# Kernel tuning notes

Hardware: AMD Instinct MI355X
Metric: run time of the kernel (lower is better)

Reference implementation:

```python
import jax, jax.numpy as jnp
import numpy as np

D_MODEL = 2048
NUM_HEADS = 16
D_K = D_MODEL // NUM_HEADS


def _xavier(key, shape):
    # xavier_uniform_ for a (fan_in, fan_out) matrix
    limit = np.sqrt(6.0 / (shape[0] + shape[1]))
    return jax.random.uniform(key, shape, dtype=jnp.float32, minval=-limit, maxval=limit)


def setup_inputs() -> dict:
    key = jax.random.key(0)
    kx, kq, kk, kv, ko = jax.random.split(key, 5)
    x = jax.random.normal(kx, (4, 2048, D_MODEL), dtype=jnp.float32)
    return {
        "x": x,
        "w_q": _xavier(kq, (D_MODEL, D_MODEL)),
        "w_k": _xavier(kk, (D_MODEL, D_MODEL)),
        "w_v": _xavier(kv, (D_MODEL, D_MODEL)),
        "w_o": _xavier(ko, (D_MODEL, D_MODEL)),
    }


def _split_heads(t):
    b, s, _ = t.shape
    return t.reshape(b, s, NUM_HEADS, D_K).transpose(0, 2, 1, 3)  # [b,h,s,dk]


def reference(x, w_q, w_k, w_v, w_o):
    q = _split_heads(x @ w_q)
    k = _split_heads(x @ w_k)
    v = _split_heads(x @ w_v)
    scale = 1.0 / np.sqrt(D_K).astype(np.float32)
    scores = jnp.einsum("bhqd,bhkd->bhqk", q, k) * scale
    attn = jax.nn.softmax(scores, axis=-1)
    out = jnp.einsum("bhqk,bhkd->bhqd", attn, v)  # [b,h,s,dk]
    b, h, s, dk = out.shape
    out = out.transpose(0, 2, 1, 3).reshape(b, s, h * dk)
    return out @ w_o
```

## Files before the change

### kernel.cpp

```cpp
#include <hip/hip_runtime.h>
#include <hip/hip_bf16.h>

typedef __attribute__((ext_vector_type(8))) __bf16 bf16x8;
typedef __attribute__((ext_vector_type(4))) float f32x4;
typedef __attribute__((ext_vector_type(16))) float f32x16;
typedef __attribute__((ext_vector_type(8))) unsigned short u16x8;
typedef unsigned short u16;

#define DEVINL static __device__ __forceinline__

namespace {
constexpr int kB = 4;
constexpr int kS = 2048;
constexpr int kDM = 2048;
constexpr int kH = 16;
constexpr int kDK = 128;
constexpr int kM = kB * kS;
constexpr int kNQKV = 3 * kDM;
constexpr float kE2 = 0.08838834764831845f * 1.44269504088896f;
}

DEVINL u16 f2bf(float f) {
  __hip_bfloat16 h = __float2bfloat16(f);
  return __builtin_bit_cast(u16, h);
}

#if __has_builtin(__builtin_amdgcn_exp2f)
DEVINL float exp2_fast(float x) { return __builtin_amdgcn_exp2f(x); }
#else
DEVINL float exp2_fast(float x) { return exp2f(x); }
#endif

#define GLOAD16(gp, lp) \
  __builtin_amdgcn_global_load_lds((const __attribute__((address_space(1))) void*)(gp), \
                                   (__attribute__((address_space(3))) void*)(lp), 16, 0, 0)

DEVINL bf16x8 lds_frag(const u16* p) { return *reinterpret_cast<const bf16x8*>(p); }

DEVINL f32x4 MFMA16x16(bf16x8 a, bf16x8 b, f32x4 c) {
  return __builtin_amdgcn_mfma_f32_16x16x32_bf16(a, b, c, 0, 0, 0);
}

struct TrueT { static constexpr bool value = true; };
struct FalseT { static constexpr bool value = false; };

__global__ __launch_bounds__(256) void cast_x_kernel(const float* __restrict__ x,
                                                     u16* __restrict__ o, int n4) {
  int i = blockIdx.x * 256 + threadIdx.x;
  if (i >= n4) return;
  float4 v = reinterpret_cast<const float4*>(x)[i];
  ushort4 r;
  r.x = f2bf(v.x); r.y = f2bf(v.y); r.z = f2bf(v.z); r.w = f2bf(v.w);
  reinterpret_cast<ushort4*>(o)[i] = r;
}

__global__ __launch_bounds__(256) void transpose_w_kernel(const float* __restrict__ w0,
    const float* __restrict__ w1, const float* __restrict__ w2, const float* __restrict__ w3,
    u16* __restrict__ wtcat, u16* __restrict__ wot) {
  const float* src = (blockIdx.z == 0) ? w0 : (blockIdx.z == 1) ? w1
                    : (blockIdx.z == 2) ? w2 : w3;
  u16* dst = (blockIdx.z < 3) ? (wtcat + (size_t)blockIdx.z * kDM * kDM) : wot;
  __shared__ float tile[32][33];
  int n0 = blockIdx.x * 32, k0 = blockIdx.y * 32;
  int tx = threadIdx.x, ty = threadIdx.y;
#pragma unroll
  for (int i = 0; i < 4; ++i)
    tile[ty + i * 8][tx] = src[(size_t)(k0 + ty + i * 8) * kDM + n0 + tx];
  __syncthreads();
#pragma unroll
  for (int i = 0; i < 4; ++i)
    dst[(size_t)(n0 + ty + i * 8) * kDM + k0 + tx] = f2bf(tile[tx][ty + i * 8]);
}

DEVINL void cstore(float* p, float v) { *p = v; }
DEVINL void cstore(u16* p, float v) { *p = f2bf(v); }

#define PH_BEGIN()                                     \
  __builtin_amdgcn_sched_barrier(0);                   \
  __builtin_amdgcn_s_barrier();                        \
  asm volatile("s_waitcnt lgkmcnt(0)" ::: "memory");   \
  __builtin_amdgcn_sched_barrier(0);                   \
  __builtin_amdgcn_s_setprio(1)

#define PH_END()                                       \
  __builtin_amdgcn_s_setprio(0);                       \
  __builtin_amdgcn_sched_barrier(0)

#define GATE4() \
  asm volatile("s_waitcnt vmcnt(4)" ::: "memory");     \
  __builtin_amdgcn_sched_barrier(0)

#define GATE0() \
  asm volatile("s_waitcnt vmcnt(0)" ::: "memory");     \
  __builtin_amdgcn_sched_barrier(0)

#define RD_A(SB, MQ, DST)                                             \
  do {                                                                \
    _Pragma("unroll") for (int mf = 0; mf < 4; ++mf) {                \
      const u16* p_ = (SB) + (awrow + (MQ) * 64 + mf * 16) * 64;      \
      DST[mf * 2 + 0] = lds_frag(p_ + g0);                            \
      DST[mf * 2 + 1] = lds_frag(p_ + g1);                            \
    }                                                                 \
  } while (0)

#define RD_BH(SB, NH)                                                 \
  do {                                                                \
    _Pragma("unroll") for (int nf = 0; nf < 2; ++nf) {                \
      const u16* p_ = (SB) + (bwrow + (NH) * 32 + nf * 16) * 64;      \
      b[(NH) * 4 + nf * 2 + 0] = lds_frag(p_ + g0);                   \
      b[(NH) * 4 + nf * 2 + 1] = lds_frag(p_ + g1);                   \
    }                                                                 \
  } while (0)

#define MMQ(MQ, NH, AF)                                               \
  do {                                                                \
    _Pragma("unroll") for (int mf = 0; mf < 4; ++mf)                  \
      _Pragma("unroll") for (int nf = 0; nf < 2; ++nf) {              \
        f32x4 t_ = acc[(MQ) * 4 + mf][(NH) * 2 + nf];                 \
        t_ = MFMA16x16(AF[mf * 2 + 0], b[(NH) * 4 + nf * 2 + 0], t_); \
        t_ = MFMA16x16(AF[mf * 2 + 1], b[(NH) * 4 + nf * 2 + 1], t_); \
        acc[(MQ) * 4 + mf][(NH) * 2 + nf] = t_;                       \
      }                                                               \
  } while (0)

#define STG_A(buf, R0, kt) \
  GLOAD16(baseA + (size_t)(R0) * lda + (size_t)(kt) * 64, ldsA + (buf) * 16384 + (R0) * 64)
#define STG_B(buf, R0, kt) \
  GLOAD16(baseB + (size_t)(R0) * ldb + (size_t)(kt) * 64, ldsB + (buf) * 16384 + (R0) * 64)

template <typename CT, bool WRITEV>
__global__ __launch_bounds__(512, 2) void gemm256_kernel(const u16* __restrict__ A,
    const u16* __restrict__ Bt, CT* __restrict__ C, u16* __restrict__ Vt,
    int K, int lda, int ldb, int ldc) {
  __shared__ __align__(16) u16 sA[2][16384];
  __shared__ __align__(16) u16 sB[2][16384];
  const int tid = threadIdx.x;
  const int lane = tid & 63, wid = tid >> 6;
  const int r15 = lane & 15, hi = lane >> 4;
  const int wm = wid >> 2, wn = wid & 3;

  const int gx = gridDim.x, nwg = gx * gridDim.y;
  const int orig = blockIdx.y * gx + blockIdx.x;
  const int wg = (orig & 7) * (nwg >> 3) + (orig >> 3);
  const int n0 = (wg % gx) * 256;
  const int m0 = (wg / gx) * 256;

  const int NT = K >> 6;
  const int NITER = NT >> 1;

  const int rc = tid >> 3;
  const int cg = (tid & 7) ^ (rc & 7);
  const u16* baseA = A + (size_t)(m0 + rc) * lda + cg * 8;
  const u16* baseB = Bt + (size_t)(n0 + rc) * ldb + cg * 8;
  u16* ldsA = &sA[0][0] + rc * 64 + (tid & 7) * 8;
  u16* ldsB = &sB[0][0] + rc * 64 + (tid & 7) * 8;

  const int sw = r15 & 7;
  const int g0 = (hi ^ sw) * 8;
  const int g1 = ((4 + hi) ^ sw) * 8;
  const int awrow = wm * 128 + r15;
  const int bwrow = wn * 64 + r15;
  const u16* sA0 = &sA[0][0]; const u16* sA1 = &sA[1][0];
  const u16* sB0 = &sB[0][0]; const u16* sB1 = &sB[1][0];

  f32x4 acc[8][4] = {};
  bf16x8 aE[8], aO[8], b[8];

  STG_A(0, 0, 0); STG_A(0, 64, 0); STG_A(0, 128, 0); STG_A(0, 192, 0);
  STG_B(0, 0, 0); STG_B(0, 64, 0); STG_B(0, 128, 0); STG_B(0, 192, 0);
  STG_A(1, 0, 1); STG_A(1, 128, 1);
  STG_B(1, 0, 1); STG_B(1, 64, 1); STG_B(1, 128, 1); STG_B(1, 192, 1);
  asm volatile("s_waitcnt vmcnt(6)" ::: "memory");
  __builtin_amdgcn_sched_barrier(0);
  __builtin_amdgcn_s_barrier();
  RD_A(sA0, 0, aE); RD_BH(sB0, 0);

  int kb = 0;
  auto iter = [&](auto lastc) {
    constexpr bool L = decltype(lastc)::value;
    const int kO = kb + 1, k2 = kb + 2, k3 = kb + 3;
    PH_BEGIN();
    RD_BH(sB0, 1);
    MMQ(0, 0, aE);
    PH_END();
    STG_A(1, 64, kO); STG_A(1, 192, kO);
    PH_BEGIN();
    RD_A(sA0, 1, aO);
    MMQ(0, 1, aE);
    PH_END();
    if constexpr (!L) { STG_A(0, 0, k2); STG_A(0, 128, k2); }
    PH_BEGIN();
    MMQ(1, 0, aO);
    PH_END();
    if constexpr (!L) { STG_B(0, 0, k2); STG_B(0, 64, k2); GATE4(); }
    else              { GATE0(); }
    PH_BEGIN();
    RD_A(sA1, 0, aE); RD_BH(sB1, 0);
    MMQ(1, 1, aO);
    PH_END();
    if constexpr (!L) { STG_B(0, 128, k2); STG_B(0, 192, k2); }
    PH_BEGIN();
    RD_BH(sB1, 1);
    MMQ(0, 0, aE);
    PH_END();
    if constexpr (!L) { STG_A(0, 64, k2); STG_A(0, 192, k2); }
    PH_BEGIN();
    RD_A(sA1, 1, aO);
    MMQ(0, 1, aE);
    PH_END();
    if constexpr (!L) { STG_A(1, 0, k3); STG_A(1, 128, k3); }
    PH_BEGIN();
    MMQ(1, 0, aO);
    PH_END();
    if constexpr (!L) { STG_B(1, 0, k3); STG_B(1, 64, k3); GATE4(); }
    else              { GATE0(); }
    PH_BEGIN();
    if constexpr (!L) { RD_A(sA0, 0, aE); RD_BH(sB0, 0); }
    MMQ(1, 1, aO);
    PH_END();
    if constexpr (!L) { STG_B(1, 128, k3); STG_B(1, 192, k3); }
    kb += 2;
  };
  for (int i = 0; i < NITER - 1; ++i) iter(FalseT{});
  iter(TrueT{});

  if constexpr (WRITEV) {
    if (n0 >= 2 * kDM) {
      const int hswap = ((hi & 1) << 1) | (hi >> 1);
#pragma unroll
      for (int im = 0; im < 8; ++im) {
        const int m_base = m0 + wm * 128 + im * 16;
        const int bq = m_base >> 11;
        const int sp = (m_base & (kS - 1)) + hswap * 4;
#pragma unroll
        for (int in = 0; in < 4; ++in) {
          const int c = n0 - 2 * kDM + wn * 64 + in * 16 + r15;
          const int hh = c >> 7, dd = c & 127;
          u16* dst = Vt + ((size_t)((bq * kH + hh) * kDK + dd)) * kS + sp;
          ushort4 pk;
          pk.x = f2bf(acc[im][in][0]); pk.y = f2bf(acc[im][in][1]);
          pk.z = f2bf(acc[im][in][2]); pk.w = f2bf(acc[im][in][3]);
          *reinterpret_cast<ushort4*>(dst) = pk;
        }
      }
      return;
    }
  }
  const size_t crow0 = (size_t)(m0 + wm * 128 + hi * 4);
  const int col0 = n0 + wn * 64 + r15;
#pragma unroll
  for (int im = 0; im < 8; ++im)
#pragma unroll
    for (int in = 0; in < 4; ++in)
#pragma unroll
      for (int r = 0; r < 4; ++r)
        cstore(&C[(crow0 + im * 16 + r) * ldc + col0 + in * 16], acc[im][in][r]);
}

__global__ __launch_bounds__(256, 2) void attn_kernel(const u16* __restrict__ qkv,
    const u16* __restrict__ vt, u16* __restrict__ attn_out) {
  __shared__ __align__(16) u16 lds[2][16384];
  const int tid = threadIdx.x;
  const int lane = tid & 63, wid = tid >> 6;
  const int l31 = lane & 31, hi5 = lane >> 5;
  const int q0 = blockIdx.x * 128, h = blockIdx.y, b = blockIdx.z;
  const int bh = b * kH + h;

  const int krow = tid >> 4, kg = tid & 15;
  const u16* kp = qkv + (size_t)(b * kS + krow) * kNQKV + kDM + h * kDK
                  + (size_t)((kg ^ (krow & 7)) * 8);
  const int vrow = tid >> 3, vg = tid & 7;
  const u16* vp = vt + (size_t)(bh * kDK + vrow) * kS + (size_t)((vg ^ (vrow & 7)) * 8);

  auto stage_kv = [&](u16* dst) {
#pragma unroll
    for (int i = 0; i < 4; ++i)
      GLOAD16(kp + (size_t)i * 16 * kNQKV, dst + (tid + 256 * i) * 8);
#pragma unroll
    for (int i = 0; i < 4; ++i)
      GLOAD16(vp + (size_t)i * 32 * kS, dst + 8192 + (tid + 256 * i) * 8);
    kp += (size_t)64 * kNQKV;
    vp += 64;
  };

#pragma unroll
  for (int i = 0; i < 8; ++i) {
    int row = (tid >> 4) + 16 * i;
    GLOAD16(qkv + (size_t)(b * kS + q0 + row) * kNQKV + h * kDK
                + (size_t)(((tid & 15) ^ (row & 7)) * 8),
            (u16*)lds[1] + (tid + 256 * i) * 8);
  }
  stage_kv(lds[0]);
  __syncthreads();

  bf16x8 qf[8];
  {
    const int qrow = wid * 32 + l31;
    const u16* qb = (const u16*)lds[1];
#pragma unroll
    for (int ds = 0; ds < 8; ++ds) {
      int slot = (ds * 2 + hi5) ^ (qrow & 7);
      qf[ds] = lds_frag(&qb[qrow * 128 + slot * 8]);
    }
  }
  __syncthreads();

  f32x16 o[4] = {};
  float mi = -1e30f, li = 0.f;
  int cur = 0;

  for (int t = 0; t < kS / 64; ++t) {
    if (t < kS / 64 - 1) stage_kv(lds[cur ^ 1]);

    const u16* Kb = (const u16*)lds[cur];
    const u16* Vb = Kb + 8192;

    f32x16 s0 = {}, s1 = {};
    const int kr = l31;
#pragma unroll
    for (int ds = 0; ds < 8; ++ds) {
      int slot = ((ds * 2 + hi5) ^ (kr & 7)) * 8;
      bf16x8 k0 = lds_frag(&Kb[kr * 128 + slot]);
      bf16x8 k1 = lds_frag(&Kb[(32 + kr) * 128 + slot]);
      s0 = __builtin_amdgcn_mfma_f32_32x32x16_bf16(k0, qf[ds], s0, 0, 0, 0);
      s1 = __builtin_amdgcn_mfma_f32_32x32x16_bf16(k1, qf[ds], s1, 0, 0, 0);
    }

    float mx = s0[0];
#pragma unroll
    for (int r = 1; r < 16; ++r) mx = fmaxf(mx, s0[r]);
#pragma unroll
    for (int r = 0; r < 16; ++r) mx = fmaxf(mx, s1[r]);
    mx = fmaxf(mx, __shfl_xor(mx, 32));
    float mc = mx * kE2;
    if (__any(mc > mi + 8.0f)) {
      float mn = fmaxf(mi, mc);
      float corr = exp2_fast(mi - mn);
      mi = mn;
      li *= corr;
#pragma unroll
      for (int r = 0; r < 16; ++r) {
        float c = __shfl(corr, (r & 3) + 8 * (r >> 2) + 4 * hi5);
        o[0][r] *= c; o[1][r] *= c; o[2][r] *= c; o[3][r] *= c;
      }
    }
    float p0[16], p1[16];
    float rs = 0.f;
#pragma unroll
    for (int r = 0; r < 16; ++r) { p0[r] = exp2_fast(s0[r] * kE2 - mi); rs += p0[r]; }
#pragma unroll
    for (int r = 0; r < 16; ++r) { p1[r] = exp2_fast(s1[r] * kE2 - mi); rs += p1[r]; }
    rs += __shfl_xor(rs, 32);
    li += rs;

    u16x8 pw0, pw1, pw2, pw3;
#pragma unroll
    for (int r = 0; r < 8; ++r) {
      pw0[r] = f2bf(p0[r]);
      pw1[r] = f2bf(p0[r + 8]);
      pw2[r] = f2bf(p1[r]);
      pw3[r] = f2bf(p1[r + 8]);
    }
    bf16x8 pa[4] = {__builtin_bit_cast(bf16x8, pw0), __builtin_bit_cast(bf16x8, pw1),
                    __builtin_bit_cast(bf16x8, pw2), __builtin_bit_cast(bf16x8, pw3)};

#pragma unroll
    for (int dt = 0; dt < 4; ++dt) {
      const int row = dt * 32 + l31;
      const int rs8 = row & 7;
#pragma unroll
      for (int ks = 0; ks < 4; ++ks) {
        bf16x8 bv = lds_frag(&Vb[row * 64 + ((ks * 2 + hi5) ^ rs8) * 8]);
        o[dt] = __builtin_amdgcn_mfma_f32_32x32x16_bf16(pa[ks], bv, o[dt], 0, 0, 0);
      }
    }

    __syncthreads();
    cur ^= 1;
  }

  float rli = 1.0f / li;
  const size_t obase = (size_t)(b * kS + q0 + wid * 32) * kDM + h * kDK + l31;
#pragma unroll
  for (int r = 0; r < 16; ++r) {
    int ql = (r & 3) + 8 * (r >> 2) + 4 * hi5;
    float w = __shfl(rli, ql);
#pragma unroll
    for (int dt = 0; dt < 4; ++dt)
      attn_out[obase + (size_t)ql * kDM + dt * 32] = f2bf(o[dt][r] * w);
  }
}

extern "C" void kernel_launch(void* const* d_in, const int* in_sizes, int n_in,
                              void* d_out, int out_size, void* d_ws, size_t ws_size,
                              hipStream_t stream) {
  (void)in_sizes; (void)n_in; (void)out_size; (void)ws_size;
  const float* x  = (const float*)d_in[0];
  const float* wq = (const float*)d_in[1];
  const float* wk = (const float*)d_in[2];
  const float* wv = (const float*)d_in[3];
  const float* wo = (const float*)d_in[4];

  char* p = (char*)d_ws;
  u16* xb   = (u16*)p; p += (size_t)kM * kDM * 2;
  u16* wtc  = (u16*)p; p += (size_t)kNQKV * kDM * 2;
  u16* wot  = (u16*)p; p += (size_t)kDM * kDM * 2;
  u16* qkvb = (u16*)p; p += (size_t)kM * kNQKV * 2;
  u16* vtb  = (u16*)p; p += (size_t)kB * kH * kDK * kS * 2;
  u16* aob  = xb;

  int n4 = kM * kDM / 4;
  cast_x_kernel<<<(n4 + 255) / 256, 256, 0, stream>>>(x, xb, n4);
  transpose_w_kernel<<<dim3(kDM / 32, kDM / 32, 4), dim3(32, 8), 0, stream>>>(
      wq, wk, wv, wo, wtc, wot);
  gemm256_kernel<u16, true><<<dim3(kNQKV / 256, kM / 256), 512, 0, stream>>>(
      xb, wtc, qkvb, vtb, kDM, kDM, kDM, kNQKV);
  attn_kernel<<<dim3(kS / 128, kH, kB), 256, 0, stream>>>(qkvb, vtb, aob);
  gemm256_kernel<float, false><<<dim3(kDM / 256, kM / 256), 512, 0, stream>>>(
      aob, wot, (float*)d_out, nullptr, kDM, kDM, kDM, kDM);
}
```

Before: 436.3 us.

## Process two 32-row query tiles per wave to reuse staged K/V tiles

Each attention block now covers 256 queries instead of 128, and each wave keeps two sets of Q fragments, accumulators and softmax stats, running the score/softmax/PV step twice per staged K/V tile. This halves K/V global-to-LDS traffic per query and halves the grid size. Q fragments are now loaded straight from global memory into registers rather than staged through LDS. The cost is much higher register pressure under launch_bounds(256,2), which risks spills, and fewer blocks (512) to fill the GPU.

```diff
diff --git a/kernel.cpp b/kernel.cpp
--- a/kernel.cpp
+++ b/kernel.cpp
@@ -263,7 +263,7 @@
   const int tid = threadIdx.x;
   const int lane = tid & 63, wid = tid >> 6;
   const int l31 = lane & 31, hi5 = lane >> 5;
-  const int q0 = blockIdx.x * 128, h = blockIdx.y, b = blockIdx.z;
+  const int q0 = blockIdx.x * 256, h = blockIdx.y, b = blockIdx.z;
   const int bh = b * kH + h;
 
   const int krow = tid >> 4, kg = tid & 15;
@@ -283,38 +283,26 @@
     vp += 64;
   };
 
-#pragma unroll
-  for (int i = 0; i < 8; ++i) {
-    int row = (tid >> 4) + 16 * i;
-    GLOAD16(qkv + (size_t)(b * kS + q0 + row) * kNQKV + h * kDK
-                + (size_t)(((tid & 15) ^ (row & 7)) * 8),
-            (u16*)lds[1] + (tid + 256 * i) * 8);
+  bf16x8 qfA[8], qfB[8];
+  {
+    const u16* qa = qkv + (size_t)(b * kS + q0 + wid * 64 + l31) * kNQKV
+                    + h * kDK + hi5 * 8;
+    const u16* qb = qa + (size_t)32 * kNQKV;
+#pragma unroll
+    for (int ds = 0; ds < 8; ++ds) {
+      qfA[ds] = *reinterpret_cast<const bf16x8*>(qa + ds * 16);
+      qfB[ds] = *reinterpret_cast<const bf16x8*>(qb + ds * 16);
+    }
   }
   stage_kv(lds[0]);
   __syncthreads();
 
-  bf16x8 qf[8];
-  {
-    const int qrow = wid * 32 + l31;
-    const u16* qb = (const u16*)lds[1];
-#pragma unroll
-    for (int ds = 0; ds < 8; ++ds) {
-      int slot = (ds * 2 + hi5) ^ (qrow & 7);
-      qf[ds] = lds_frag(&qb[qrow * 128 + slot * 8]);
-    }
-  }
-  __syncthreads();
-
-  f32x16 o[4] = {};
-  float mi = -1e30f, li = 0.f;
+  f32x16 oA[4] = {}, oB[4] = {};
+  float miA = -1e30f, liA = 0.f, miB = -1e30f, liB = 0.f;
   int cur = 0;
 
-  for (int t = 0; t < kS / 64; ++t) {
-    if (t < kS / 64 - 1) stage_kv(lds[cur ^ 1]);
-
-    const u16* Kb = (const u16*)lds[cur];
-    const u16* Vb = Kb + 8192;
-
+  auto process = [&](const u16* Kb, const u16* Vb, bf16x8* qf, f32x16* o,
+                     float& mi, float& li) {
     f32x16 s0 = {}, s1 = {};
     const int kr = l31;
 #pragma unroll
@@ -374,20 +362,32 @@
         o[dt] = __builtin_amdgcn_mfma_f32_32x32x16_bf16(pa[ks], bv, o[dt], 0, 0, 0);
       }
     }
+  };
+
+  for (int t = 0; t < kS / 64; ++t) {
+    if (t < kS / 64 - 1) stage_kv(lds[cur ^ 1]);
+
+    const u16* Kb = (const u16*)lds[cur];
+    const u16* Vb = Kb + 8192;
+    process(Kb, Vb, qfA, oA, miA, liA);
+    process(Kb, Vb, qfB, oB, miB, liB);
 
     __syncthreads();
     cur ^= 1;
   }
 
-  float rli = 1.0f / li;
-  const size_t obase = (size_t)(b * kS + q0 + wid * 32) * kDM + h * kDK + l31;
+  const size_t obase = (size_t)(b * kS + q0 + wid * 64) * kDM + h * kDK + l31;
+  float rliA = 1.0f / liA, rliB = 1.0f / liB;
 #pragma unroll
   for (int r = 0; r < 16; ++r) {
     int ql = (r & 3) + 8 * (r >> 2) + 4 * hi5;
-    float w = __shfl(rli, ql);
-#pragma unroll
-    for (int dt = 0; dt < 4; ++dt)
-      attn_out[obase + (size_t)ql * kDM + dt * 32] = f2bf(o[dt][r] * w);
+    float wA = __shfl(rliA, ql);
+    float wB = __shfl(rliB, ql);
+#pragma unroll
+    for (int dt = 0; dt < 4; ++dt) {
+      attn_out[obase + (size_t)ql * kDM + dt * 32] = f2bf(oA[dt][r] * wA);
+      attn_out[obase + (size_t)(32 + ql) * kDM + dt * 32] = f2bf(oB[dt][r] * wB);
+    }
   }
 }
 
@@ -415,7 +415,7 @@
       wq, wk, wv, wo, wtc, wot);
   gemm256_kernel<u16, true><<<dim3(kNQKV / 256, kM / 256), 512, 0, stream>>>(
       xb, wtc, qkvb, vtb, kDM, kDM, kDM, kNQKV);
-  attn_kernel<<<dim3(kS / 128, kH, kB), 256, 0, stream>>>(qkvb, vtb, aob);
+  attn_kernel<<<dim3(kS / 256, kH, kB), 256, 0, stream>>>(qkvb, vtb, aob);
   gemm256_kernel<float, false><<<dim3(kDM / 256, kM / 256), 512, 0, stream>>>(
       aob, wot, (float*)d_out, nullptr, kDM, kDM, kDM, kDM);
 }
```

New measurement: 822.5 us. 88.5% more time.

## Single-buffer V in LDS and raise attention occupancy to three blocks per CU

Applied to the files above, without the earlier changes.

The attention kernel's LDS shrinks from 64KB to 48KB by double-buffering only K and keeping V in a single buffer that is loaded at the start of each iteration. Launch bounds go from 2 to 3 blocks per CU. Manual vmcnt waits and s_barriers let the QK^T/softmax phase start before V has arrived, with V awaited only before the PV matmul. The costs are tighter register limits under 3-block occupancy, which could cause spills, and V loads that are less hidden because they overlap only the current tile's compute.

```diff
diff --git a/kernel.cpp b/kernel.cpp
--- a/kernel.cpp
+++ b/kernel.cpp
@@ -257,9 +257,10 @@
         cstore(&C[(crow0 + im * 16 + r) * ldc + col0 + in * 16], acc[im][in][r]);
 }
 
-__global__ __launch_bounds__(256, 2) void attn_kernel(const u16* __restrict__ qkv,
+__global__ __launch_bounds__(256, 3) void attn_kernel(const u16* __restrict__ qkv,
     const u16* __restrict__ vt, u16* __restrict__ attn_out) {
-  __shared__ __align__(16) u16 lds[2][16384];
+  __shared__ __align__(16) u16 ldsK[2][8192];
+  __shared__ __align__(16) u16 ldsV[8192];
   const int tid = threadIdx.x;
   const int lane = tid & 63, wid = tid >> 6;
   const int l31 = lane & 31, hi5 = lane >> 5;
@@ -272,14 +273,16 @@
   const int vrow = tid >> 3, vg = tid & 7;
   const u16* vp = vt + (size_t)(bh * kDK + vrow) * kS + (size_t)((vg ^ (vrow & 7)) * 8);
 
-  auto stage_kv = [&](u16* dst) {
+  auto stage_k = [&](u16* dst) {
 #pragma unroll
     for (int i = 0; i < 4; ++i)
       GLOAD16(kp + (size_t)i * 16 * kNQKV, dst + (tid + 256 * i) * 8);
+    kp += (size_t)64 * kNQKV;
+  };
+  auto stage_v = [&]() {
 #pragma unroll
     for (int i = 0; i < 4; ++i)
-      GLOAD16(vp + (size_t)i * 32 * kS, dst + 8192 + (tid + 256 * i) * 8);
-    kp += (size_t)64 * kNQKV;
+      GLOAD16(vp + (size_t)i * 32 * kS, &ldsV[0] + (tid + 256 * i) * 8);
     vp += 64;
   };
 
@@ -288,33 +291,36 @@
     int row = (tid >> 4) + 16 * i;
     GLOAD16(qkv + (size_t)(b * kS + q0 + row) * kNQKV + h * kDK
                 + (size_t)(((tid & 15) ^ (row & 7)) * 8),
-            (u16*)lds[1] + (tid + 256 * i) * 8);
+            &ldsK[0][0] + (tid + 256 * i) * 8);
   }
-  stage_kv(lds[0]);
   __syncthreads();
 
   bf16x8 qf[8];
   {
     const int qrow = wid * 32 + l31;
-    const u16* qb = (const u16*)lds[1];
 #pragma unroll
     for (int ds = 0; ds < 8; ++ds) {
       int slot = (ds * 2 + hi5) ^ (qrow & 7);
-      qf[ds] = lds_frag(&qb[qrow * 128 + slot * 8]);
+      qf[ds] = lds_frag(&ldsK[0][0] + qrow * 128 + slot * 8);
     }
   }
   __syncthreads();
+  stage_k(&ldsK[0][0]);
 
   f32x16 o[4] = {};
   float mi = -1e30f, li = 0.f;
   int cur = 0;
 
   for (int t = 0; t < kS / 64; ++t) {
-    if (t < kS / 64 - 1) stage_kv(lds[cur ^ 1]);
-
-    const u16* Kb = (const u16*)lds[cur];
-    const u16* Vb = Kb + 8192;
-
+    stage_v();
+    if (t < kS / 64 - 1) stage_k(&ldsK[cur ^ 1][0]);
+
+    if (t < kS / 64 - 1) { asm volatile("s_waitcnt vmcnt(8)" ::: "memory"); }
+    else                 { asm volatile("s_waitcnt vmcnt(4)" ::: "memory"); }
+    __builtin_amdgcn_sched_barrier(0);
+    __builtin_amdgcn_s_barrier();
+
+    const u16* Kb = &ldsK[cur][0];
     f32x16 s0 = {}, s1 = {};
     const int kr = l31;
 #pragma unroll
@@ -364,18 +370,24 @@
     bf16x8 pa[4] = {__builtin_bit_cast(bf16x8, pw0), __builtin_bit_cast(bf16x8, pw1),
                     __builtin_bit_cast(bf16x8, pw2), __builtin_bit_cast(bf16x8, pw3)};
 
+    if (t < kS / 64 - 1) { asm volatile("s_waitcnt vmcnt(4)" ::: "memory"); }
+    else                 { asm volatile("s_waitcnt vmcnt(0)" ::: "memory"); }
+    __builtin_amdgcn_sched_barrier(0);
+    __builtin_amdgcn_s_barrier();
+
 #pragma unroll
     for (int dt = 0; dt < 4; ++dt) {
       const int row = dt * 32 + l31;
       const int rs8 = row & 7;
 #pragma unroll
       for (int ks = 0; ks < 4; ++ks) {
-        bf16x8 bv = lds_frag(&Vb[row * 64 + ((ks * 2 + hi5) ^ rs8) * 8]);
+        bf16x8 bv = lds_frag(&ldsV[row * 64 + ((ks * 2 + hi5) ^ rs8) * 8]);
         o[dt] = __builtin_amdgcn_mfma_f32_32x32x16_bf16(pa[ks], bv, o[dt], 0, 0, 0);
       }
     }
 
-    __syncthreads();
+    __builtin_amdgcn_sched_barrier(0);
+    __builtin_amdgcn_s_barrier();
     cur ^= 1;
   }
 
```

Measured after the change: 446.5 us. 1.02x slower.
